# Optimization experiments

Hardware: AMD Instinct MI355X
Metric: run time of the kernel (lower is better)

## Reference

```python
import jax, jax.numpy as jnp
import numpy as np

D_MODEL = 768; D_STATE = 64; D_CONV = 4; EXPAND = 2
D_INNER = EXPAND * D_MODEL            # 1536
HEADDIM = 64; NHEADS = D_INNER // HEADDIM  # 24
NGROUPS = 1
CONV_DIM = D_INNER + 2 * NGROUPS * D_STATE        # 1664
D_IN_PROJ = 2 * D_INNER + 2 * NGROUPS * D_STATE + NHEADS  # 3224
B_SZ = 2; SEQ = 4096
EPS = 1e-5


def setup_inputs() -> dict:
    key = jax.random.key(0)
    ks = jax.random.split(key, 10)
    s = 0.02
    return {
        "x": jax.random.normal(ks[0], (B_SZ, SEQ, D_MODEL), jnp.float32),
        "ln_w": jnp.ones((D_MODEL,), jnp.float32),
        "ln_b": jnp.zeros((D_MODEL,), jnp.float32),
        "in_proj_w": jax.random.normal(ks[1], (D_MODEL, D_IN_PROJ), jnp.float32) * s,
        "conv_w": jax.random.normal(ks[2], (CONV_DIM, D_CONV), jnp.float32) * s,
        "conv_b": jnp.zeros((CONV_DIM,), jnp.float32),
        "dt_bias": jax.random.uniform(ks[3], (NHEADS,), jnp.float32, -4.6, -2.0),
        "A_log": jnp.log(jnp.arange(1, NHEADS + 1, dtype=jnp.float32)),
        "D_param": jnp.ones((NHEADS,), jnp.float32),
        "rms_w": jnp.ones((D_INNER,), jnp.float32),
        "out_proj_w": jax.random.normal(ks[4], (D_INNER, D_MODEL), jnp.float32) * s,
        "gate_w": jax.random.normal(ks[5], (D_MODEL, D_MODEL), jnp.float32) * s,
        "gate_b": jnp.zeros((D_MODEL,), jnp.float32),
        "out_w": jax.random.normal(ks[6], (D_MODEL, D_MODEL), jnp.float32) * s,
        "out_b": jnp.zeros((D_MODEL,), jnp.float32),
    }


def _silu(u):
    return u * jax.nn.sigmoid(u)


def _causal_conv1d(x, w, b):
    # x: [B,L,C], w: [C,K] depthwise, left-padded causal conv
    K = w.shape[1]
    L = x.shape[1]
    xp = jnp.pad(x, ((0, 0), (K - 1, 0), (0, 0)))
    y = b
    for k in range(K):
        y = y + xp[:, k:k + L, :] * w[:, k]
    return y


def _selective_scan(xh, dt, A, Bm, Cm):
    # xh: [B,L,H,P], dt: [B,L,H], A: [H], Bm/Cm: [B,L,N] (ngroups=1)
    dA = jnp.exp(dt * A)  # [B,L,H]
    # time-major for scan
    dA_t = jnp.moveaxis(dA, 1, 0)            # [L,B,H]
    dt_t = jnp.moveaxis(dt, 1, 0)            # [L,B,H]
    x_t = jnp.moveaxis(xh, 1, 0)             # [L,B,H,P]
    B_t = jnp.moveaxis(Bm, 1, 0)             # [L,B,N]
    C_t = jnp.moveaxis(Cm, 1, 0)             # [L,B,N]

    h0 = jnp.zeros((xh.shape[0], NHEADS, HEADDIM, D_STATE), xh.dtype)

    def step(h, inp):
        da, dtv, xv, bv, cv = inp
        # dBx: [B,H,P,N] built per-step to avoid materializing [B,L,H,P,N]
        dBx = (dtv[:, :, None] * xv)[..., None] * bv[:, None, None, :]
        h = h * da[:, :, None, None] + dBx
        y = jnp.einsum('bhpn,bn->bhp', h, cv)
        return h, y

    _, ys = jax.lax.scan(step, h0, (dA_t, dt_t, x_t, B_t, C_t))
    return jnp.moveaxis(ys, 0, 1)  # [B,L,H,P]


def _mamba2(xn, in_proj_w, conv_w, conv_b, dt_bias, A_log, D_param, rms_w, out_proj_w):
    zxbcdt = xn @ in_proj_w  # [B,L,D_IN_PROJ]
    z = zxbcdt[..., :D_INNER]
    xBC = zxbcdt[..., D_INNER:D_INNER + CONV_DIM]
    dt = zxbcdt[..., D_INNER + CONV_DIM:]

    xBC = _silu(_causal_conv1d(xBC, conv_w, conv_b))
    xh = xBC[..., :D_INNER]
    Bm = xBC[..., D_INNER:D_INNER + NGROUPS * D_STATE]
    Cm = xBC[..., D_INNER + NGROUPS * D_STATE:]

    dt = jax.nn.softplus(dt + dt_bias)        # [B,L,H]
    A = -jnp.exp(A_log)                       # [H]

    B, L = xh.shape[0], xh.shape[1]
    xh = xh.reshape(B, L, NHEADS, HEADDIM)
    y = _selective_scan(xh, dt, A, Bm, Cm)
    y = y + xh * D_param[None, None, :, None]  # skip connection D*x
    y = y.reshape(B, L, D_INNER)

    # gated RMSNorm: rmsnorm(y * silu(z)) * w
    y = y * _silu(z)
    y = y * jax.lax.rsqrt(jnp.mean(y * y, axis=-1, keepdims=True) + EPS) * rms_w
    return y @ out_proj_w


def reference(x, ln_w, ln_b, in_proj_w, conv_w, conv_b, dt_bias, A_log, D_param,
              rms_w, out_proj_w, gate_w, gate_b, out_w, out_b):
    mu = jnp.mean(x, axis=-1, keepdims=True)
    var = jnp.mean((x - mu) ** 2, axis=-1, keepdims=True)
    x_norm = (x - mu) * jax.lax.rsqrt(var + EPS) * ln_w + ln_b

    y = _mamba2(x_norm, in_proj_w, conv_w, conv_b, dt_bias, A_log, D_param, rms_w, out_proj_w)
    gate = jax.nn.sigmoid(x_norm @ gate_w + gate_b)
    y_gated = y * gate
    return x + y_gated @ out_w + out_b
```

## Files before the change

kernel.cpp:

```cpp
#include <hip/hip_runtime.h>
#include <hip/hip_bf16.h>
#include <cstddef>

#define DMODEL  768
#define DINNER  1536
#define DSTATE  64
#define NH      24
#define HD      64
#define CONVD   1664
#define DINPROJ 3224
#define SEQ     4096
#define BSZ     2
#define NTOK    8192
#define NCHUNK  64
#define EPSF    1e-5f
#define LP      72
#define BUFS    8192

typedef __attribute__((ext_vector_type(8))) short  short8;
typedef __attribute__((ext_vector_type(4))) float  f32x4;

__device__ __forceinline__ unsigned short f2bf(float f) {
  union { float f; unsigned int u; } v; v.f = f;
  unsigned int r = v.u + 0x7fffu + ((v.u >> 16) & 1u);
  return (unsigned short)(r >> 16);
}
__device__ __forceinline__ float bf2f(unsigned short u) {
  union { unsigned int i; float f; } v; v.i = ((unsigned int)u) << 16; return v.f;
}
__device__ __forceinline__ unsigned long long pack4bf(float a, float b, float c, float d) {
  return (unsigned long long)(f2bf(a) | ((unsigned int)f2bf(b) << 16))
       | ((unsigned long long)(f2bf(c) | ((unsigned int)f2bf(d) << 16)) << 32);
}
__device__ __forceinline__ float sigm(float x) { return 1.f / (1.f + __expf(-x)); }

__device__ __forceinline__ void gld16(const unsigned short* g, unsigned short* l) {
  __builtin_amdgcn_global_load_lds(
      (const __attribute__((address_space(1))) unsigned int*)g,
      (__attribute__((address_space(3))) unsigned int*)l, 16, 0, 0);
}

__device__ __forceinline__ void xcd_tiles(int& m0, int& n0) {
  const int nt = gridDim.x, mt = gridDim.y;
  const int id = blockIdx.y * nt + blockIdx.x;
  const int mper = mt >> 3;
  const int xcd = id & 7, within = id >> 3;
  m0 = (xcd * mper + (within % mper)) * 128;
  n0 = (within / mper) * 128;
}

__global__ __launch_bounds__(256) void k_ln(const float* __restrict__ x,
    const float* __restrict__ w, const float* __restrict__ b,
    unsigned short* __restrict__ xn)
{
  __shared__ float red[4];
  const int row = blockIdx.x, tid = threadIdx.x;
  const float* xr = x + (size_t)row * DMODEL;
  float v[3]; float s = 0.f;
  #pragma unroll
  for (int q = 0; q < 3; q++) { v[q] = xr[q*256 + tid]; s += v[q]; }
  #pragma unroll
  for (int off = 32; off; off >>= 1) s += __shfl_down(s, off);
  if ((tid & 63) == 0) red[tid >> 6] = s;
  __syncthreads();
  const float mu = (red[0] + red[1] + red[2] + red[3]) * (1.f / DMODEL);
  __syncthreads();
  float s2 = 0.f;
  #pragma unroll
  for (int q = 0; q < 3; q++) { float d = v[q] - mu; s2 += d * d; }
  #pragma unroll
  for (int off = 32; off; off >>= 1) s2 += __shfl_down(s2, off);
  if ((tid & 63) == 0) red[tid >> 6] = s2;
  __syncthreads();
  const float rs = rsqrtf((red[0] + red[1] + red[2] + red[3]) * (1.f / DMODEL) + EPSF);
  unsigned short* xo = xn + (size_t)row * DMODEL;
  #pragma unroll
  for (int q = 0; q < 3; q++) {
    int col = q*256 + tid;
    xo[col] = f2bf((v[q] - mu) * rs * w[col] + b[col]);
  }
}

__global__ __launch_bounds__(256) void k_wtrans4(
    const float* __restrict__ W0, unsigned short* __restrict__ T0,
    const float* __restrict__ W1, unsigned short* __restrict__ T1,
    const float* __restrict__ W2, unsigned short* __restrict__ T2,
    const float* __restrict__ W3, unsigned short* __restrict__ T3)
{
  const float* W; unsigned short* T; int K, N;
  switch (blockIdx.z) {
    case 0:  W = W0; T = T0; K = 768;  N = 3224; break;
    case 1:  W = W1; T = T1; K = 768;  N = 768;  break;
    case 2:  W = W2; T = T2; K = 1536; N = 768;  break;
    default: W = W3; T = T3; K = 768;  N = 768;  break;
  }
  const int n0 = blockIdx.x * 32, k0 = blockIdx.y * 32;
  if (n0 >= N || k0 >= K) return;
  __shared__ float tile[32][33];
  const int tid = threadIdx.x;
  const int tx = tid & 31, ty = tid >> 5;
  #pragma unroll
  for (int r = 0; r < 4; r++) {
    int k = k0 + ty + 8*r;
    if (k < K && n0 + tx < N) tile[ty + 8*r][tx] = W[(size_t)k * N + n0 + tx];
  }
  __syncthreads();
  #pragma unroll
  for (int r = 0; r < 4; r++) {
    int n = n0 + ty + 8*r, k = k0 + tx;
    if (n < N && k < K) T[(size_t)n * K + k] = f2bf(tile[tx][ty + 8*r]);
  }
}

__device__ __forceinline__ void gemm_core(const unsigned short* __restrict__ A,
    const unsigned short* __restrict__ Bt, float* __restrict__ C,
    unsigned short* __restrict__ Cb,
    int M, int N, int K, int epi, const float* __restrict__ bias,
    const float* __restrict__ resid, int m0, int n0,
    unsigned short* As, unsigned short* Bs)
{
  const int tid = threadIdx.x;
  const int lane = tid & 63, w = tid >> 6;
  const int wm = (w >> 1) * 64, wn = (w & 1) * 64;
  const int l15 = lane & 15, lq = lane >> 4;
  const int sw = l15 & 7;
  f32x4 acc[4][4];
  #pragma unroll
  for (int i = 0; i < 4; i++)
    #pragma unroll
    for (int j = 0; j < 4; j++) acc[i][j] = (f32x4){0.f, 0.f, 0.f, 0.f};

  int rowg[4], gq[4], nrg[4];
  #pragma unroll
  for (int r = 0; r < 4; r++) {
    int gi = (r * 4 + w) * 64 + lane;
    rowg[r] = gi >> 3;
    gq[r] = (gi & 7) ^ (rowg[r] & 7);
    int nr = n0 + rowg[r]; if (nr >= N) nr = N - 1;
    nrg[r] = nr;
  }

  #pragma unroll
  for (int r = 0; r < 4; r++)
    gld16(A + (size_t)(m0 + rowg[r]) * K + gq[r] * 8, &As[(r * 4 + w) * 512]);
  #pragma unroll
  for (int r = 0; r < 4; r++)
    gld16(Bt + (size_t)nrg[r] * K + gq[r] * 8, &Bs[(r * 4 + w) * 512]);

  int p = 0;
  for (int k0 = 0; k0 < K; k0 += 64) {
    __syncthreads();
    if (k0 + 64 < K) {
      const int pn = p ^ 1;
      #pragma unroll
      for (int r = 0; r < 4; r++)
        gld16(A + (size_t)(m0 + rowg[r]) * K + (k0 + 64) + gq[r] * 8,
              &As[pn * BUFS + (r * 4 + w) * 512]);
      #pragma unroll
      for (int r = 0; r < 4; r++)
        gld16(Bt + (size_t)nrg[r] * K + (k0 + 64) + gq[r] * 8,
              &Bs[pn * BUFS + (r * 4 + w) * 512]);
    }
    const unsigned short* Ab = As + p * BUFS;
    const unsigned short* Bb = Bs + p * BUFS;
    #pragma unroll
    for (int ks = 0; ks < 2; ks++) {
      short8 a8[4], b8[4];
      #pragma unroll
      for (int mi = 0; mi < 4; mi++)
        a8[mi] = *(const short8*)(&Ab[(wm + 16 * mi + l15) * 64 + ((lq + 4 * ks) ^ sw) * 8]);
      #pragma unroll
      for (int ni = 0; ni < 4; ni++)
        b8[ni] = *(const short8*)(&Bb[(wn + 16 * ni + l15) * 64 + ((lq + 4 * ks) ^ sw) * 8]);
      #pragma unroll
      for (int mi = 0; mi < 4; mi++)
        #pragma unroll
        for (int ni = 0; ni < 4; ni++)
          acc[mi][ni] = __builtin_amdgcn_mfma_f32_16x16x32_bf16(a8[mi], b8[ni], acc[mi][ni], 0, 0, 0);
    }
    p ^= 1;
  }
  #pragma unroll
  for (int mi = 0; mi < 4; mi++) {
    #pragma unroll
    for (int r = 0; r < 4; r++) {
      int row = m0 + wm + 16*mi + lq*4 + r;
      #pragma unroll
      for (int ni = 0; ni < 4; ni++) {
        int col = n0 + wn + 16*ni + l15;
        if (col < N) {
          float vv = acc[mi][ni][r];
          if (epi == 1)      vv = sigm(vv + bias[col]);
          else if (epi == 2) vv = vv + bias[col] + resid[(size_t)row * N + col];
          if (Cb) Cb[(size_t)row * N + col] = f2bf(vv);
          else    C [(size_t)row * N + col] = vv;
        }
      }
    }
  }
}

__global__ __launch_bounds__(256) void k_gemm(const unsigned short* __restrict__ A,
    const unsigned short* __restrict__ Bt, float* __restrict__ C,
    unsigned short* __restrict__ Cb,
    int M, int N, int K, int epi, const float* __restrict__ bias,
    const float* __restrict__ resid)
{
  __shared__ alignas(16) unsigned short As[2 * BUFS];
  __shared__ alignas(16) unsigned short Bs[2 * BUFS];
  int m0, n0;
  xcd_tiles(m0, n0);
  gemm_core(A, Bt, C, Cb, M, N, K, epi, bias, resid, m0, n0, As, Bs);
}

__global__ __launch_bounds__(256) void k_dualgemm(
    const unsigned short* __restrict__ A0, const unsigned short* __restrict__ B0,
    unsigned short* __restrict__ C0, int K0,
    const unsigned short* __restrict__ A1, const unsigned short* __restrict__ B1,
    unsigned short* __restrict__ C1, int K1, const float* __restrict__ bias1, int N)
{
  __shared__ alignas(16) unsigned short As[2 * BUFS];
  __shared__ alignas(16) unsigned short Bs[2 * BUFS];
  int m0, n0;
  xcd_tiles(m0, n0);
  if (blockIdx.z == 0)
    gemm_core(A0, B0, nullptr, C0, NTOK, N, K0, 0, nullptr, nullptr, m0, n0, As, Bs);
  else
    gemm_core(A1, B1, nullptr, C1, NTOK, N, K1, 1, bias1, nullptr, m0, n0, As, Bs);
}

__global__ __launch_bounds__(256) void k_conv(const unsigned short* __restrict__ zx,
    const float* __restrict__ cw, const float* __restrict__ cb,
    unsigned short* __restrict__ out)
{
  __shared__ alignas(8) unsigned short tile[67][132];
  const int tid = threadIdx.x;
  const int c0 = blockIdx.x * 128;
  const int tc = blockIdx.y;
  const int t0 = tc * 64;
  const bool haloOK = (tc & 63) != 0;
  for (int i = tid; i < 67 * 16; i += 256) {
    int row = i >> 4, g = i & 15;
    unsigned long long v0 = 0, v1 = 0;
    if (row >= 3 || haloOK) {
      const unsigned short* p = zx + (size_t)(t0 - 3 + row) * DINPROJ + DINNER + c0 + g * 8;
      v0 = *(const unsigned long long*)p;
      v1 = *(const unsigned long long*)(p + 4);
    }
    *(unsigned long long*)(&tile[row][g * 8])     = v0;
    *(unsigned long long*)(&tile[row][g * 8 + 4]) = v1;
  }
  __syncthreads();
  const int ch0 = (tid & 63) * 2;
  const int trow = tid >> 6;
  const int cg = c0 + ch0;
  float cw0[4], cw1[4];
  #pragma unroll
  for (int k = 0; k < 4; k++) { cw0[k] = cw[cg * 4 + k]; cw1[k] = cw[(cg + 1) * 4 + k]; }
  const float cb0 = cb[cg], cb1 = cb[cg + 1];
  #pragma unroll
  for (int q = 0; q < 16; q++) {
    int tq = trow * 16 + q;
    float a0 = cb0, a1 = cb1;
    #pragma unroll
    for (int k = 0; k < 4; k++) {
      unsigned int u = *(const unsigned int*)(&tile[tq + k][ch0]);
      a0 += bf2f((unsigned short)u) * cw0[k];
      a1 += bf2f((unsigned short)(u >> 16)) * cw1[k];
    }
    float s0 = a0 * sigm(a0), s1 = a1 * sigm(a1);
    *(unsigned int*)(out + (size_t)(t0 + tq) * CONVD + cg) =
        (unsigned int)f2bf(s0) | ((unsigned int)f2bf(s1) << 16);
  }
}

__global__ __launch_bounds__(256) void k_chunkstate(const unsigned short* __restrict__ zx,
    const unsigned short* __restrict__ xbcc, const float* __restrict__ dt_bias,
    const float* __restrict__ A_log, float* __restrict__ S, float* __restrict__ CD)
{
  const int c = blockIdx.x, bh = blockIdx.y;
  const int b = bh / NH, h = bh % NH;
  const int tid = threadIdx.x;
  const int lane = tid & 63, w = tid >> 6;
  const int l15 = lane & 15, lq = lane >> 4;
  __shared__ float wv_[64];
  __shared__ alignas(16) unsigned short Bwt[64][LP];
  __shared__ alignas(16) unsigned short Xt [64][LP];

  if (tid < 64) {
    int t = c * 64 + tid;
    float xx = bf2f(zx[((size_t)(b * SEQ + t)) * DINPROJ + (DINNER + CONVD) + h]) + dt_bias[h];
    float dt_ = (xx > 15.f) ? xx : log1pf(__expf(xx));
    float Ah = -__expf(A_log[h]);
    float v = dt_ * Ah;
    #pragma unroll
    for (int off = 1; off < 64; off <<= 1) {
      float u = __shfl_up(v, off);
      if (tid >= off) v += u;
    }
    float L63 = __shfl(v, 63);
    wv_[tid] = __expf(L63 - v) * dt_;
    if (tid == 63) CD[bh * 64 + c] = __expf(v);
  }
  unsigned long long braw[4];
  #pragma unroll
  for (int it = 0; it < 4; it++) {
    int i4 = tid + 256 * it;
    int s = i4 >> 4, q4 = (i4 & 15) * 4;
    size_t rb = ((size_t)(b * SEQ) + c * 64 + s) * CONVD;
    braw[it] = *(const unsigned long long*)(xbcc + rb + DINNER + q4);
    unsigned short xs[4];
    *(unsigned long long*)xs = *(const unsigned long long*)(xbcc + rb + h * HD + q4);
    Xt[q4+0][s] = xs[0]; Xt[q4+1][s] = xs[1]; Xt[q4+2][s] = xs[2]; Xt[q4+3][s] = xs[3];
  }
  __syncthreads();
  #pragma unroll
  for (int it = 0; it < 4; it++) {
    int i4 = tid + 256 * it;
    int s = i4 >> 4, q4 = (i4 & 15) * 4;
    float wsc = wv_[s];
    unsigned short us[4];
    *(unsigned long long*)us = braw[it];
    Bwt[q4+0][s] = f2bf(bf2f(us[0]) * wsc);
    Bwt[q4+1][s] = f2bf(bf2f(us[1]) * wsc);
    Bwt[q4+2][s] = f2bf(bf2f(us[2]) * wsc);
    Bwt[q4+3][s] = f2bf(bf2f(us[3]) * wsc);
  }
  __syncthreads();
  const int n0 = 16 * w;
  short8 a0 = *(const short8*)(&Bwt[n0 + l15][lq * 8]);
  short8 a1 = *(const short8*)(&Bwt[n0 + l15][32 + lq * 8]);
  size_t sb = ((size_t)bh * 64 + c) * 4096;
  #pragma unroll
  for (int pt = 0; pt < 4; pt++) {
    f32x4 acc = (f32x4){0.f, 0.f, 0.f, 0.f};
    short8 b0 = *(const short8*)(&Xt[16*pt + l15][lq * 8]);
    short8 b1 = *(const short8*)(&Xt[16*pt + l15][32 + lq * 8]);
    acc = __builtin_amdgcn_mfma_f32_16x16x32_bf16(a0, b0, acc, 0, 0, 0);
    acc = __builtin_amdgcn_mfma_f32_16x16x32_bf16(a1, b1, acc, 0, 0, 0);
    #pragma unroll
    for (int r = 0; r < 4; r++) {
      int n = n0 + 4*lq + r, p = 16*pt + l15;
      S[sb + (size_t)n * 64 + p] = acc[r];
    }
  }
}

__global__ __launch_bounds__(256) void k_chunkrec(float* __restrict__ S,
    const float* __restrict__ CD)
{
  const int bh = blockIdx.x >> 4, part = blockIdx.x & 15;
  const int e = part * 256 + threadIdx.x;
  float g = 0.f;
  size_t base = (size_t)bh * 64 * 4096 + e;
  for (int c = 0; c < 64; c++) {
    size_t ad = base + (size_t)c * 4096;
    float sv = S[ad];
    float pc = CD[bh * 64 + c];
    S[ad] = g;
    g = pc * g + sv;
  }
}

__global__ __launch_bounds__(256) void k_chunkout(const unsigned short* __restrict__ zx,
    const unsigned short* __restrict__ xbcc, const float* __restrict__ S,
    const float* __restrict__ dt_bias, const float* __restrict__ A_log,
    const float* __restrict__ Dp, unsigned short* __restrict__ Y)
{
  const int c = blockIdx.x, bh = blockIdx.y;
  const int b = bh / NH, h = bh % NH;
  const int tid = threadIdx.x;
  const int lane = tid & 63, w = tid >> 6;
  const int l15 = lane & 15, lq = lane >> 4;
  __shared__ float dts[64], Lc[64], ein[64];
  __shared__ alignas(16) unsigned short Cs  [64][LP];
  __shared__ alignas(16) unsigned short BsPs[64][LP];
  __shared__ alignas(16) unsigned short Xt  [64][LP];
  __shared__ alignas(16) unsigned short Gt  [64][LP];

  if (tid < 64) {
    int t = c * 64 + tid;
    float xx = bf2f(zx[((size_t)(b * SEQ + t)) * DINPROJ + (DINNER + CONVD) + h]) + dt_bias[h];
    float dt_ = (xx > 15.f) ? xx : log1pf(__expf(xx));
    dts[tid] = dt_;
    float Ah = -__expf(A_log[h]);
    float v = dt_ * Ah;
    #pragma unroll
    for (int off = 1; off < 64; off <<= 1) {
      float u = __shfl_up(v, off);
      if (tid >= off) v += u;
    }
    Lc[tid] = v;
    ein[tid] = __expf(v);
  }
  const size_t gslot = ((size_t)bh * 64 + c) * 4096;
  #pragma unroll
  for (int it = 0; it < 4; it++) {
    int i4 = tid + 256 * it;
    int rr = i4 >> 4, q4 = (i4 & 15) * 4;
    size_t rb = ((size_t)(b * SEQ) + c * 64 + rr) * CONVD;
    const unsigned short* pC = xbcc + rb + (DINNER + DSTATE) + q4;
    Cs[rr][q4+0] = pC[0]; Cs[rr][q4+1] = pC[1]; Cs[rr][q4+2] = pC[2]; Cs[rr][q4+3] = pC[3];
    const unsigned short* pB = xbcc + rb + DINNER + q4;
    BsPs[rr][q4+0] = pB[0]; BsPs[rr][q4+1] = pB[1]; BsPs[rr][q4+2] = pB[2]; BsPs[rr][q4+3] = pB[3];
    unsigned short xs[4];
    *(unsigned long long*)xs = *(const unsigned long long*)(xbcc + rb + h * HD + q4);
    Xt[q4+0][rr] = xs[0]; Xt[q4+1][rr] = xs[1]; Xt[q4+2][rr] = xs[2]; Xt[q4+3][rr] = xs[3];
    float4 vG = *(const float4*)(S + gslot + (size_t)i4 * 4);
    Gt[q4+0][rr] = f2bf(vG.x); Gt[q4+1][rr] = f2bf(vG.y);
    Gt[q4+2][rr] = f2bf(vG.z); Gt[q4+3][rr] = f2bf(vG.w);
  }
  __syncthreads();
  const int i0 = 16 * w;
  short8 ac0 = *(const short8*)(&Cs[i0 + l15][lq * 8]);
  short8 ac1 = *(const short8*)(&Cs[i0 + l15][32 + lq * 8]);
  float pp[4][4];
  #pragma unroll
  for (int st = 0; st < 4; st++) {
    f32x4 g = (f32x4){0.f, 0.f, 0.f, 0.f};
    if (st <= w) {
      short8 b0 = *(const short8*)(&BsPs[16*st + l15][lq * 8]);
      short8 b1 = *(const short8*)(&BsPs[16*st + l15][32 + lq * 8]);
      g = __builtin_amdgcn_mfma_f32_16x16x32_bf16(ac0, b0, g, 0, 0, 0);
      g = __builtin_amdgcn_mfma_f32_16x16x32_bf16(ac1, b1, g, 0, 0, 0);
    }
    #pragma unroll
    for (int r = 0; r < 4; r++) {
      int i = i0 + 4*lq + r, s = 16*st + l15;
      pp[st][r] = (s <= i) ? g[r] * __expf(Lc[i] - Lc[s]) * dts[s] : 0.f;
    }
  }
  __syncthreads();
  #pragma unroll
  for (int st = 0; st < 4; st++)
    #pragma unroll
    for (int r = 0; r < 4; r++)
      BsPs[i0 + 4*lq + r][16*st + l15] = f2bf(pp[st][r]);
  __syncthreads();
  short8 ap0 = *(const short8*)(&BsPs[i0 + l15][lq * 8]);
  short8 ap1 = *(const short8*)(&BsPs[i0 + l15][32 + lq * 8]);
  const float Dh = Dp[h];
  #pragma unroll
  for (int pt = 0; pt < 4; pt++) {
    const int p0 = 16 * pt;
    f32x4 y1 = (f32x4){0.f, 0.f, 0.f, 0.f};
    f32x4 y2 = (f32x4){0.f, 0.f, 0.f, 0.f};
    short8 bx0 = *(const short8*)(&Xt[p0 + l15][lq * 8]);
    y1 = __builtin_amdgcn_mfma_f32_16x16x32_bf16(ap0, bx0, y1, 0, 0, 0);
    if (w >= 2) {
      short8 bx1 = *(const short8*)(&Xt[p0 + l15][32 + lq * 8]);
      y1 = __builtin_amdgcn_mfma_f32_16x16x32_bf16(ap1, bx1, y1, 0, 0, 0);
    }
    short8 bg0 = *(const short8*)(&Gt[p0 + l15][lq * 8]);
    short8 bg1 = *(const short8*)(&Gt[p0 + l15][32 + lq * 8]);
    y2 = __builtin_amdgcn_mfma_f32_16x16x32_bf16(ac0, bg0, y2, 0, 0, 0);
    y2 = __builtin_amdgcn_mfma_f32_16x16x32_bf16(ac1, bg1, y2, 0, 0, 0);
    #pragma unroll
    for (int r = 0; r < 4; r++) {
      int i = i0 + 4*lq + r, p = p0 + l15;
      float xv = bf2f(Xt[p][i]);
      float o = y1[r] + ein[i] * y2[r] + Dh * xv;
      Y[((size_t)(b * SEQ) + c * 64 + i) * DINNER + h * HD + p] = f2bf(o);
    }
  }
}

__global__ __launch_bounds__(256) void k_fuse(const unsigned short* __restrict__ Y,
    const unsigned short* __restrict__ ZX, const float* __restrict__ rw,
    unsigned short* __restrict__ YN)
{
  __shared__ float red[4];
  const int row = blockIdx.x, tid = threadIdx.x;
  const unsigned short* yr = Y + (size_t)row * DINNER;
  const unsigned short* zr = ZX + (size_t)row * DINPROJ;
  float v[6]; float s2 = 0.f;
  #pragma unroll
  for (int q = 0; q < 6; q++) {
    int col = q * 256 + tid;
    float z = bf2f(zr[col]);
    float yv = bf2f(yr[col]) * (z * sigm(z));
    v[q] = yv; s2 += yv * yv;
  }
  #pragma unroll
  for (int off = 32; off; off >>= 1) s2 += __shfl_down(s2, off);
  if ((tid & 63) == 0) red[tid >> 6] = s2;
  __syncthreads();
  const float rs = rsqrtf((red[0] + red[1] + red[2] + red[3]) * (1.f / DINNER) + EPSF);
  unsigned short* yo = YN + (size_t)row * DINNER;
  #pragma unroll
  for (int q = 0; q < 6; q++) {
    int col = q * 256 + tid;
    yo[col] = f2bf(v[q] * rs * rw[col]);
  }
}

__global__ __launch_bounds__(256) void k_gatemul(const unsigned short* __restrict__ YP,
    const unsigned short* __restrict__ G, unsigned short* __restrict__ YG)
{
  size_t i4 = ((size_t)blockIdx.x * 256 + threadIdx.x) * 4;
  unsigned short a[4], b[4];
  *(unsigned long long*)a = *(const unsigned long long*)(YP + i4);
  *(unsigned long long*)b = *(const unsigned long long*)(G + i4);
  *(unsigned long long*)(YG + i4) = pack4bf(
      bf2f(a[0]) * bf2f(b[0]), bf2f(a[1]) * bf2f(b[1]),
      bf2f(a[2]) * bf2f(b[2]), bf2f(a[3]) * bf2f(b[3]));
}

extern "C" void kernel_launch(void* const* d_in, const int* in_sizes, int n_in,
                              void* d_out, int out_size, void* d_ws, size_t ws_size,
                              hipStream_t stream)
{
  const float* x         = (const float*)d_in[0];
  const float* ln_w      = (const float*)d_in[1];
  const float* ln_b      = (const float*)d_in[2];
  const float* in_proj_w = (const float*)d_in[3];
  const float* conv_w    = (const float*)d_in[4];
  const float* conv_b    = (const float*)d_in[5];
  const float* dt_bias   = (const float*)d_in[6];
  const float* A_log     = (const float*)d_in[7];
  const float* D_param   = (const float*)d_in[8];
  const float* rms_w     = (const float*)d_in[9];
  const float* out_proj_w= (const float*)d_in[10];
  const float* gate_w    = (const float*)d_in[11];
  const float* gate_b    = (const float*)d_in[12];
  const float* out_w     = (const float*)d_in[13];
  const float* out_b     = (const float*)d_in[14];
  float* out = (float*)d_out;
  char* ws = (char*)d_ws;

  const size_t WS_NEEDED = 177848320ull;
  if (ws_size < WS_NEEDED) return;

  unsigned short* XN    = (unsigned short*)(ws + 0);
  unsigned short* WIT   = (unsigned short*)(ws + 12582912);
  unsigned short* WGT   = (unsigned short*)(ws + 17534976);
  unsigned short* WOPT  = (unsigned short*)(ws + 18714624);
  unsigned short* WOT   = (unsigned short*)(ws + 21073920);
  unsigned short* ZXb   = (unsigned short*)(ws + 22253568);
  unsigned short* XBCCb = (unsigned short*)(ws + 75075584);
  float*          SG    = (float*)(ws + 102338560);
  float*          CD    = (float*)(ws + 152670208);
  unsigned short* Yb    = (unsigned short*)(ws + 152682496);
  unsigned short* YN    = (unsigned short*)(ws + 102338560);
  unsigned short* Gb    = (unsigned short*)(ws + 22253568);
  unsigned short* YPb   = (unsigned short*)(ws + 34836480);
  unsigned short* YG    = (unsigned short*)(ws + 75075584);

  k_wtrans4<<<dim3(101, 48, 4), 256, 0, stream>>>(in_proj_w, WIT, gate_w, WGT,
                                                  out_proj_w, WOPT, out_w, WOT);
  k_ln<<<NTOK, 256, 0, stream>>>(x, ln_w, ln_b, XN);
  k_gemm<<<dim3(26, 64), 256, 0, stream>>>(XN, WIT, nullptr, ZXb, NTOK, DINPROJ, DMODEL, 0, nullptr, nullptr);
  k_conv<<<dim3(13, 128), 256, 0, stream>>>(ZXb, conv_w, conv_b, XBCCb);
  k_chunkstate<<<dim3(NCHUNK, BSZ * NH), 256, 0, stream>>>(ZXb, XBCCb, dt_bias, A_log, SG, CD);
  k_chunkrec<<<BSZ * NH * 16, 256, 0, stream>>>(SG, CD);
  k_chunkout<<<dim3(NCHUNK, BSZ * NH), 256, 0, stream>>>(ZXb, XBCCb, SG, dt_bias, A_log, D_param, Yb);
  k_fuse<<<NTOK, 256, 0, stream>>>(Yb, ZXb, rms_w, YN);
  k_dualgemm<<<dim3(6, 64, 2), 256, 0, stream>>>(YN, WOPT, YPb, DINNER,
                                                 XN, WGT, Gb, DMODEL, gate_b, DMODEL);
  k_gatemul<<<(NTOK * DMODEL / 4) / 256, 256, 0, stream>>>(YPb, Gb, YG);
  k_gemm<<<dim3(6, 64), 256, 0, stream>>>(YG, WOT, out, nullptr, NTOK, DMODEL, DMODEL, 2, out_b, x);
}
```

Measured before the change: 395.9 us.

## Fuse gate GEMM into in_proj launch and store chunk states as bf16

The gate projection (XN @ gate_w) now shares one launch with the in_proj GEMM, since both read XN. Blocks are tiled per XCD, 208 in_proj tiles plus 48 gate tiles per XCD, and the gate output moves to its own workspace slot. The out_proj GEMM now runs alone. Chunk states are stored as bf16 instead of fp32, which halves the traffic through chunkstate, chunkrec and chunkout. The cost is lower precision in the inter-chunk recurrence, because the running states are rounded to bf16 when stored.

```diff
diff --git a/kernel.cpp b/kernel.cpp
--- a/kernel.cpp
+++ b/kernel.cpp
@@ -213,20 +213,26 @@
   gemm_core(A, Bt, C, Cb, M, N, K, epi, bias, resid, m0, n0, As, Bs);
 }
 
-__global__ __launch_bounds__(256) void k_dualgemm(
-    const unsigned short* __restrict__ A0, const unsigned short* __restrict__ B0,
-    unsigned short* __restrict__ C0, int K0,
-    const unsigned short* __restrict__ A1, const unsigned short* __restrict__ B1,
-    unsigned short* __restrict__ C1, int K1, const float* __restrict__ bias1, int N)
+__global__ __launch_bounds__(256) void k_ipg(
+    const unsigned short* __restrict__ XN, const unsigned short* __restrict__ WIT,
+    unsigned short* __restrict__ ZXb,
+    const unsigned short* __restrict__ WGT, unsigned short* __restrict__ Gb,
+    const float* __restrict__ gate_b)
 {
   __shared__ alignas(16) unsigned short As[2 * BUFS];
   __shared__ alignas(16) unsigned short Bs[2 * BUFS];
-  int m0, n0;
-  xcd_tiles(m0, n0);
-  if (blockIdx.z == 0)
-    gemm_core(A0, B0, nullptr, C0, NTOK, N, K0, 0, nullptr, nullptr, m0, n0, As, Bs);
-  else
-    gemm_core(A1, B1, nullptr, C1, NTOK, N, K1, 1, bias1, nullptr, m0, n0, As, Bs);
+  const int id = blockIdx.x;
+  const int xcd = id & 7, within = id >> 3;
+  if (within < 208) {
+    int m0 = (xcd * 8 + (within & 7)) * 128;
+    int n0 = (within >> 3) * 128;
+    gemm_core(XN, WIT, nullptr, ZXb, NTOK, DINPROJ, DMODEL, 0, nullptr, nullptr, m0, n0, As, Bs);
+  } else {
+    int w2 = within - 208;
+    int m0 = (xcd * 8 + (w2 & 7)) * 128;
+    int n0 = (w2 >> 3) * 128;
+    gemm_core(XN, WGT, nullptr, Gb, NTOK, DMODEL, DMODEL, 1, gate_b, nullptr, m0, n0, As, Bs);
+  }
 }
 
 __global__ __launch_bounds__(256) void k_conv(const unsigned short* __restrict__ zx,
@@ -276,7 +282,7 @@
 
 __global__ __launch_bounds__(256) void k_chunkstate(const unsigned short* __restrict__ zx,
     const unsigned short* __restrict__ xbcc, const float* __restrict__ dt_bias,
-    const float* __restrict__ A_log, float* __restrict__ S, float* __restrict__ CD)
+    const float* __restrict__ A_log, unsigned short* __restrict__ S, float* __restrict__ CD)
 {
   const int c = blockIdx.x, bh = blockIdx.y;
   const int b = bh / NH, h = bh % NH;
@@ -341,12 +347,12 @@
     #pragma unroll
     for (int r = 0; r < 4; r++) {
       int n = n0 + 4*lq + r, p = 16*pt + l15;
-      S[sb + (size_t)n * 64 + p] = acc[r];
-    }
-  }
-}
-
-__global__ __launch_bounds__(256) void k_chunkrec(float* __restrict__ S,
+      S[sb + (size_t)n * 64 + p] = f2bf(acc[r]);
+    }
+  }
+}
+
+__global__ __launch_bounds__(256) void k_chunkrec(unsigned short* __restrict__ S,
     const float* __restrict__ CD)
 {
   const int bh = blockIdx.x >> 4, part = blockIdx.x & 15;
@@ -355,15 +361,15 @@
   size_t base = (size_t)bh * 64 * 4096 + e;
   for (int c = 0; c < 64; c++) {
     size_t ad = base + (size_t)c * 4096;
-    float sv = S[ad];
+    float sv = bf2f(S[ad]);
     float pc = CD[bh * 64 + c];
-    S[ad] = g;
+    S[ad] = f2bf(g);
     g = pc * g + sv;
   }
 }
 
 __global__ __launch_bounds__(256) void k_chunkout(const unsigned short* __restrict__ zx,
-    const unsigned short* __restrict__ xbcc, const float* __restrict__ S,
+    const unsigned short* __restrict__ xbcc, const unsigned short* __restrict__ S,
     const float* __restrict__ dt_bias, const float* __restrict__ A_log,
     const float* __restrict__ Dp, unsigned short* __restrict__ Y)
 {
@@ -406,9 +412,9 @@
     unsigned short xs[4];
     *(unsigned long long*)xs = *(const unsigned long long*)(xbcc + rb + h * HD + q4);
     Xt[q4+0][rr] = xs[0]; Xt[q4+1][rr] = xs[1]; Xt[q4+2][rr] = xs[2]; Xt[q4+3][rr] = xs[3];
-    float4 vG = *(const float4*)(S + gslot + (size_t)i4 * 4);
-    Gt[q4+0][rr] = f2bf(vG.x); Gt[q4+1][rr] = f2bf(vG.y);
-    Gt[q4+2][rr] = f2bf(vG.z); Gt[q4+3][rr] = f2bf(vG.w);
+    unsigned short gs[4];
+    *(unsigned long long*)gs = *(const unsigned long long*)(S + gslot + (size_t)i4 * 4);
+    Gt[q4+0][rr] = gs[0]; Gt[q4+1][rr] = gs[1]; Gt[q4+2][rr] = gs[2]; Gt[q4+3][rr] = gs[3];
   }
   __syncthreads();
   const int i0 = 16 * w;
@@ -538,25 +544,24 @@
   unsigned short* WOT   = (unsigned short*)(ws + 21073920);
   unsigned short* ZXb   = (unsigned short*)(ws + 22253568);
   unsigned short* XBCCb = (unsigned short*)(ws + 75075584);
-  float*          SG    = (float*)(ws + 102338560);
+  unsigned short* Sb    = (unsigned short*)(ws + 102338560);
+  unsigned short* Gb    = (unsigned short*)(ws + 127504384);
   float*          CD    = (float*)(ws + 152670208);
   unsigned short* Yb    = (unsigned short*)(ws + 152682496);
   unsigned short* YN    = (unsigned short*)(ws + 102338560);
-  unsigned short* Gb    = (unsigned short*)(ws + 22253568);
   unsigned short* YPb   = (unsigned short*)(ws + 34836480);
   unsigned short* YG    = (unsigned short*)(ws + 75075584);
 
   k_wtrans4<<<dim3(101, 48, 4), 256, 0, stream>>>(in_proj_w, WIT, gate_w, WGT,
                                                   out_proj_w, WOPT, out_w, WOT);
   k_ln<<<NTOK, 256, 0, stream>>>(x, ln_w, ln_b, XN);
-  k_gemm<<<dim3(26, 64), 256, 0, stream>>>(XN, WIT, nullptr, ZXb, NTOK, DINPROJ, DMODEL, 0, nullptr, nullptr);
+  k_ipg<<<2048, 256, 0, stream>>>(XN, WIT, ZXb, WGT, Gb, gate_b);
   k_conv<<<dim3(13, 128), 256, 0, stream>>>(ZXb, conv_w, conv_b, XBCCb);
-  k_chunkstate<<<dim3(NCHUNK, BSZ * NH), 256, 0, stream>>>(ZXb, XBCCb, dt_bias, A_log, SG, CD);
-  k_chunkrec<<<BSZ * NH * 16, 256, 0, stream>>>(SG, CD);
-  k_chunkout<<<dim3(NCHUNK, BSZ * NH), 256, 0, stream>>>(ZXb, XBCCb, SG, dt_bias, A_log, D_param, Yb);
+  k_chunkstate<<<dim3(NCHUNK, BSZ * NH), 256, 0, stream>>>(ZXb, XBCCb, dt_bias, A_log, Sb, CD);
+  k_chunkrec<<<BSZ * NH * 16, 256, 0, stream>>>(Sb, CD);
+  k_chunkout<<<dim3(NCHUNK, BSZ * NH), 256, 0, stream>>>(ZXb, XBCCb, Sb, dt_bias, A_log, D_param, Yb);
   k_fuse<<<NTOK, 256, 0, stream>>>(Yb, ZXb, rms_w, YN);
-  k_dualgemm<<<dim3(6, 64, 2), 256, 0, stream>>>(YN, WOPT, YPb, DINNER,
-                                                 XN, WGT, Gb, DMODEL, gate_b, DMODEL);
+  k_gemm<<<dim3(6, 64), 256, 0, stream>>>(YN, WOPT, nullptr, YPb, NTOK, DMODEL, DINNER, 0, nullptr, nullptr);
   k_gatemul<<<(NTOK * DMODEL / 4) / 256, 256, 0, stream>>>(YPb, Gb, YG);
   k_gemm<<<dim3(6, 64), 256, 0, stream>>>(YG, WOT, out, nullptr, NTOK, DMODEL, DMODEL, 2, out_b, x);
 }
```

New measurement: 367.9 us. 1.08x faster.
